# Kernel tuning notes

Hardware: AMD Instinct MI355X
Metric: run time of the kernel (lower is better)

## Reference

```python
import jax, jax.numpy as jnp
import numpy as np

BN_EPS = 1e-5

def conv1x1(x, w, b):
    # x: [N,C,T,V], w: [O,C], b: [O]
    return jnp.einsum('nctv,oc->notv', x, w) + b[None, :, None, None]

def conv9(x, w, b):
    # (9,1) temporal conv, padding (4,0). x: [N,C,T,V], w: [O,C,9], b: [O]
    out = jax.lax.conv_general_dilated(
        x, w[:, :, :, None], window_strides=(1, 1), padding=((4, 4), (0, 0)),
        dimension_numbers=('NCHW', 'OIHW', 'NCHW'))
    return out + b[None, :, None, None]

def attn_adj(f1, f2):
    # f1,f2: [N,inter,T,V] -> softmax over rows (axis -2) of [N,V,V]
    N, ic, T, V = f1.shape
    a1 = jnp.transpose(f1, (0, 3, 1, 2)).reshape(N, V, ic * T)  # permute(0,3,1,2).view
    a2 = f2.reshape(N, ic * T, V)
    scores = jnp.einsum('nvk,nkw->nvw', a1, a2) / (ic * T)
    return jax.nn.softmax(scores, axis=-2)


def setup_inputs() -> dict:
    key = jax.random.key(0)
    ks = jax.random.split(key, 16)
    N, C, T, V, S, IC = 16, 256, 64, 25, 3, 64
    s = lambda k, shape, sc=0.05: jax.random.normal(k, shape, dtype=jnp.float32) * sc
    return {
        'x': jax.random.normal(ks[0], (N, C, T, V), dtype=jnp.float32),
        'A': jax.random.uniform(ks[1], (S, V, V), dtype=jnp.float32),
        'PA': s(ks[2], (S, V, V), 1e-3),
        'wa': s(ks[3], (S, IC, C)), 'ba': jnp.zeros((S, IC), jnp.float32),
        'wb': s(ks[4], (S, IC, C)), 'bb': jnp.zeros((S, IC), jnp.float32),
        'wT1': s(ks[5], (S, IC, C, 9)), 'bT1': jnp.zeros((S, IC), jnp.float32),
        'wT2': s(ks[6], (S, IC, C, 9)), 'bT2': jnp.zeros((S, IC), jnp.float32),
        'wST11': s(ks[7], (S, IC, C, 9)), 'bST11': jnp.zeros((S, IC), jnp.float32),
        'wST12': s(ks[8], (S, IC, C, 9)), 'bST12': jnp.zeros((S, IC), jnp.float32),
        'wd': s(ks[9], (S, C, C)), 'bd': jnp.zeros((S, C), jnp.float32),
        'gamma': jnp.ones((C,), jnp.float32), 'beta': jnp.zeros((C,), jnp.float32),
        'bn_mean': jnp.zeros((C,), jnp.float32), 'bn_var': jnp.ones((C,), jnp.float32),
    }


def reference(x, A, PA, wa, ba, wb, bb, wT1, bT1, wT2, bT2,
              wST11, bST11, wST12, bST12, wd, bd, gamma, beta, bn_mean, bn_var):
    N, C, T, V = x.shape
    I = jnp.eye(V, dtype=x.dtype)
    # Chebyshev-like static graph transforms (computed once in __init__ in torch)
    A_ch4s = jax.nn.softmax((8 * A**4 - 4 * A**2 - 4 * A + I) / V, axis=-2)
    A_ch3 = 4 * A**2 - A - 2 * I
    A_all = A_ch3 + A_ch4s + PA  # [3,V,V]

    xf = x.reshape(N, C * T, V)
    y = 0.0
    for i in range(3):
        A1 = attn_adj(conv1x1(x, wa[i], ba[i]), conv1x1(x, wb[i], bb[i]))
        AT = attn_adj(conv9(x, wT1[i], bT1[i]), conv9(x, wT2[i], bT2[i]))
        # ModuleList append quirk: even i -> 1x1 conv (center tap), odd i -> (9,1) conv
        if i % 2 == 0:
            s1 = conv1x1(x, wST11[i, :, :, 4], bST11[i])
            s2 = conv1x1(x, wST12[i, :, :, 4], bST12[i])
        else:
            s1 = conv9(x, wST11[i], bST11[i])
            s2 = conv9(x, wST12[i], bST12[i])
        AST = attn_adj(s1, s2)
        Ai = A_all[i] + A1 + AT + AST  # [N,V,V]
        z = jnp.einsum('nkv,nvw->nkw', xf, Ai).reshape(N, C, T, V)
        y = y + conv1x1(z, wd[i], bd[i])

    yb = (y - bn_mean[None, :, None, None]) * (gamma[None, :, None, None]
         / jnp.sqrt(bn_var[None, :, None, None] + BN_EPS)) + beta[None, :, None, None]
    return jax.nn.relu(yb + x)  # down is identity (in_channels == out_channels)
```

## Files before the change

kernel.cpp:

```cpp
#include <hip/hip_runtime.h>
#include <hip/hip_bf16.h>

#define NN 16
#define CC 256
#define TT 64
#define VV 25
#define ICC 64
#define TV 1600
#define CTV 409600
#define NICTV 1638400

typedef __bf16 v8bf __attribute__((ext_vector_type(8)));
typedef __bf16 v4bf __attribute__((ext_vector_type(4)));
typedef float f32x16 __attribute__((ext_vector_type(16)));

struct ConvPairs {
  const __bf16* wA[5];
  const __bf16* wB[5];
  const float*  bA[5];
  const float*  bB[5];
};

__device__ __forceinline__ void gl_lds16(const __bf16* g, __bf16* l){
  __builtin_amdgcn_global_load_lds(
      (const __attribute__((address_space(1))) unsigned int*)g,
      (__attribute__((address_space(3))) unsigned int*)l, 16, 0, 0);
}

__global__ __launch_bounds__(256) void prep_k(
    const float* __restrict__ x, __bf16* __restrict__ xt,
    const float* __restrict__ wT1, const float* __restrict__ wT2,
    const float* __restrict__ wST11, const float* __restrict__ wST12,
    __bf16* __restrict__ wT1p, __bf16* __restrict__ wT2p,
    __bf16* __restrict__ wS1p, __bf16* __restrict__ wS2p,
    const float* __restrict__ wa, const float* __restrict__ wb,
    __bf16* __restrict__ wabp, __bf16* __restrict__ wScp,
    const float* __restrict__ wd, __bf16* __restrict__ wdb,
    const float* __restrict__ A, const float* __restrict__ PA,
    float* __restrict__ Aall, __bf16* __restrict__ zp){
  __shared__ __align__(16) float smf[64*65];
  __bf16* smb = (__bf16*)smf;
  int b = blockIdx.x;
  int tid = threadIdx.x;
  if (b < 64){
    int t = b >> 3, ch64 = (b >> 1) & 3, o2 = b & 1;
    const float* src; __bf16* dst;
    if (t < 3)      { src = wT1  + (size_t)t*147456;     dst = wT1p + (size_t)t*147456; }
    else if (t < 6) { src = wT2  + (size_t)(t-3)*147456; dst = wT2p + (size_t)(t-3)*147456; }
    else if (t == 6){ src = wST11 + 147456;              dst = wS1p; }
    else            { src = wST12 + 147456;              dst = wS2p; }
    const float* in = src + (size_t)(o2*32)*2304 + ch64*576;
    for (int i = tid; i < 32*576; i += 256){
      int row = i / 576, cc = i % 576;
      smb[i] = (__bf16)in[(size_t)row*2304 + cc];
    }
    __syncthreads();
    for (int i = tid; i < 18432; i += 256){
      int e = i & 7, l = (i >> 3) & 63, ks = (i >> 9) & 1;
      int r10 = i >> 10;
      int tap = r10 % 9, chh = r10 / 9;
      int ol = l & 31, hh = l >> 5;
      int cl = ks*16 + hh*8 + e;
      int c64 = chh*32 + cl;
      int ch8 = ch64*2 + chh;
      dst[(size_t)((((ch8*9 + tap)*2 + ks)*2 + o2)*512) + l*8 + e]
          = smb[ol*576 + c64*9 + tap];
    }
  } else if (b < 74){
    int u = b - 64;
    for (int it = 0; it < 8; ++it){
      int i = tid + it*256;
      int e = i & 7, l = (i >> 3) & 63, o2 = (i >> 9) & 1;
      int ks = (i >> 10) & 1, ch = i >> 11;
      int ol = l & 31, hh = l >> 5;
      int o = o2*32 + ol;
      int c = ch*32 + ks*16 + hh*8 + e;
      __bf16 v;
      if (u < 6){
        const float* w = (u < 3) ? (wa + (size_t)u*16384) : (wb + (size_t)(u-3)*16384);
        v = (__bf16)w[(size_t)o*256 + c];
      } else {
        int i9 = ((u == 6) || (u == 8)) ? 0 : 2;
        const float* w = ((u < 8) ? wST11 : wST12) + (size_t)i9*147456;
        v = (__bf16)w[((size_t)o*256 + c)*9 + 4];
      }
      __bf16* dst = (u < 6) ? (wabp + (size_t)u*16384) : (wScp + (size_t)(u-6)*16384);
      dst[i] = v;
    }
  } else if (b < 842){
    int i = (b-74)*256 + tid;
    if (i < 196608) wdb[i] = (__bf16)wd[i];
  } else if (b == 842){
    int t = tid;
    if (t < 75){
      int s = t / 25, w = t % 25;
      float a[25], m[25];
      float mx = -3.4e38f;
      for (int v = 0; v < 25; ++v){
        float av = A[(s*25 + v)*25 + w];
        a[v] = av;
        float d = (v == w) ? 1.f : 0.f;
        float mm = (8.f*av*av*av*av - 4.f*av*av - 4.f*av + d) * 0.04f;
        m[v] = mm;
        mx = fmaxf(mx, mm);
      }
      float sum = 0.f;
      for (int v = 0; v < 25; ++v){ float e = __expf(m[v]-mx); m[v] = e; sum += e; }
      float inv = 1.f/sum;
      for (int v = 0; v < 25; ++v){
        float av = a[v];
        float d = (v == w) ? 1.f : 0.f;
        Aall[(s*25+v)*25 + w] = m[v]*inv + 4.f*av*av - av - 2.f*d + PA[(s*25+v)*25+w];
      }
    } else if (t >= 128){
      zp[t-128] = (__bf16)0.f;
    }
  } else {
    int idx = b - 843;
    int p0 = (idx % 25)*64, c0 = ((idx/25) & 3)*64, n = idx/100;
    for (int i = tid; i < 4096; i += 256){
      int cc = i >> 6, pp = i & 63;
      smf[cc*65+pp] = x[(size_t)n*CTV + (size_t)(c0+cc)*TV + p0 + pp];
    }
    __syncthreads();
    for (int i = tid; i < 4096; i += 256){
      int pp = i >> 6, cc = i & 63;
      xt[((size_t)n*TV + p0+pp)*256 + c0+cc] = (__bf16)smf[cc*65+pp];
    }
  }
}

template<int NTAPS>
__global__ __launch_bounds__(512, 2) void conv13_k(const __bf16* __restrict__ xt,
    ConvPairs cp, const __bf16* __restrict__ zp, __bf16* __restrict__ fbuf){
  extern __shared__ __bf16 sm[];
  constexpr int HALO  = (NTAPS==9) ? 100 : 0;
  constexpr int NROWS = 512 + 2*HALO;
  constexpr int SLOTS = NROWS*4;
  constexpr int KSTG  = (SLOTS + 511)/512;
  constexpr int NSTEP = NTAPS*2;
  constexpr int AD    = (NSTEP >= 4) ? 4 : 2;
  int p0 = blockIdx.x*512;
  int n  = blockIdx.y;
  int pr = blockIdx.z;
  int tid = threadIdx.x;
  int lane = tid & 63;
  int wave = tid >> 6;
  int which = wave >> 2, wq = wave & 3;
  int h = lane >> 5, l31 = lane & 31;
  const __bf16* wp = (which ? cp.wB[pr] : cp.wA[pr]) + lane*8;
  const __bf16* xtn = xt + (size_t)n*CTV;
  __bf16* buf0 = sm;
  __bf16* buf1 = sm + NROWS*32;

  f32x16 acc[2][4];
  #pragma unroll
  for (int a=0;a<2;++a)
    #pragma unroll
    for (int b=0;b<4;++b)
      #pragma unroll
      for (int r=0;r<16;++r) acc[a][b][r] = 0.f;

  int rowbase = wq*128 + l31;

  auto stage = [&](__bf16* bn, int ch){
    #pragma unroll
    for (int k=0; k<KSTG; ++k){
      int slot = k*512 + tid;
      if ((SLOTS & 511) && slot >= SLOTS) continue;
      const __bf16* src;
      if (NTAPS == 1){
        int l31s = slot & 31, f = slot >> 5;
        int h_ = f & 1, ks_ = (f >> 1) & 1, pblk = f >> 2;
        int pg = p0 + pblk*32 + l31s;
        src = (pg < 1600) ? (xtn + (size_t)pg*256 + ch*32 + ks_*16 + h_*8)
                          : zp;
      } else {
        int row = slot >> 2, g2 = slot & 3;
        int g = (g2 - (row>>1)) & 3;
        int pg = p0 - HALO + row;
        src = ((unsigned)pg < 1600u) ? (xtn + (size_t)pg*256 + ch*32 + g*8)
                                     : zp;
      }
      gl_lds16(src, bn + (size_t)slot*8);
    }
  };
  auto ldA = [&](int ch, int s, v8bf* aa){
    int tap = s >> 1, ks = s & 1;
    size_t o = (size_t)(((ch*NTAPS + tap)*2 + ks)*2)*512;
    aa[0] = *(const v8bf*)(wp + o);
    aa[1] = *(const v8bf*)(wp + o + 512);
  };
  auto ldB = [&](const __bf16* bc, int s, v8bf* bb){
    int tap = s >> 1, ks = s & 1;
    #pragma unroll
    for (int pq=0; pq<4; ++pq){
      if (NTAPS == 1){
        int frag = ((wq*4 + pq)*2 + ks)*2 + h;
        bb[pq] = *(const v8bf*)(bc + frag*256 + l31*8);
      } else {
        int row = tap*25 + rowbase + pq*32;
        int gs = ((ks*2 + h) + (row>>1)) & 3;
        bb[pq] = *(const v8bf*)(bc + row*32 + gs*8);
      }
    }
  };

  v8bf ar[AD][2];
  #pragma unroll
  for (int i=0; i<AD; ++i) ldA(0, i, ar[i]);
  stage(buf0, 0);
  __syncthreads();

  for (int ch=0; ch<8; ++ch){
    const __bf16* bc = (ch & 1) ? buf1 : buf0;
    __bf16*       bn = (ch & 1) ? buf0 : buf1;
    if (ch < 7) stage(bn, ch+1);
    v8bf bR[2][4];
    ldB(bc, 0, bR[0]);
    ldB(bc, 1, bR[1]);
    #pragma unroll
    for (int s=0; s<NSTEP; ++s){
      int cb = s & 1;
      int ca = s & (AD-1);
      v8bf A0 = ar[ca][0], A1 = ar[ca][1];
      v8bf B0 = bR[cb][0], B1 = bR[cb][1], B2 = bR[cb][2], B3 = bR[cb][3];
      if (s+2 < NSTEP) ldB(bc, s+2, bR[cb]);
      if (s+AD < NSTEP)      ldA(ch, s+AD, ar[ca]);
      else if (ch < 7)       ldA(ch+1, s+AD-NSTEP, ar[ca]);
      __builtin_amdgcn_s_setprio(1);
      acc[0][0] = __builtin_amdgcn_mfma_f32_32x32x16_bf16(A0, B0, acc[0][0], 0,0,0);
      acc[1][0] = __builtin_amdgcn_mfma_f32_32x32x16_bf16(A1, B0, acc[1][0], 0,0,0);
      acc[0][1] = __builtin_amdgcn_mfma_f32_32x32x16_bf16(A0, B1, acc[0][1], 0,0,0);
      acc[1][1] = __builtin_amdgcn_mfma_f32_32x32x16_bf16(A1, B1, acc[1][1], 0,0,0);
      acc[0][2] = __builtin_amdgcn_mfma_f32_32x32x16_bf16(A0, B2, acc[0][2], 0,0,0);
      acc[1][2] = __builtin_amdgcn_mfma_f32_32x32x16_bf16(A1, B2, acc[1][2], 0,0,0);
      acc[0][3] = __builtin_amdgcn_mfma_f32_32x32x16_bf16(A0, B3, acc[0][3], 0,0,0);
      acc[1][3] = __builtin_amdgcn_mfma_f32_32x32x16_bf16(A1, B3, acc[1][3], 0,0,0);
      __builtin_amdgcn_s_setprio(0);
    }
    __syncthreads();
  }

  const float* bias = which ? cp.bB[pr] : cp.bA[pr];
  __bf16* outb = fbuf + (size_t)(pr*2 + which)*NICTV + (size_t)n*TV*64;
  #pragma unroll
  for (int pq=0; pq<4; ++pq){
    int p = p0 + wq*128 + pq*32 + l31;
    if (p >= 1600) continue;
    __bf16* orow = outb + (size_t)p*64;
    #pragma unroll
    for (int of=0; of<2; ++of){
      #pragma unroll
      for (int g=0; g<4; ++g){
        int og = of*32 + 8*g + 4*h;
        v4bf pk;
        #pragma unroll
        for (int j=0;j<4;++j) pk[j] = (__bf16)(acc[of][pq][4*g+j] + bias[og+j]);
        *(v4bf*)(orow + og) = pk;
      }
    }
  }
}

__global__ __launch_bounds__(256, 2) void ugemm6_k(const __bf16* __restrict__ xt,
    const __bf16* __restrict__ wdb, __bf16* __restrict__ ubuf){
  __shared__ __bf16 sm[64*256];
  int p0 = blockIdx.x*64;
  int n  = blockIdx.y;
  int tid = threadIdx.x;
  int lane = tid & 63;
  int os = tid >> 6;
  int h = lane >> 5, l31 = lane & 31;
  const __bf16* xtn = xt + (size_t)n*CTV;

  for (int s2 = tid; s2 < 64*32; s2 += 256){
    int row = s2 >> 5, g = s2 & 31;
    uint4 val = *(const uint4*)(xtn + (size_t)(p0+row)*256 + g*8);
    int gs = (g + row) & 31;
    *(uint4*)(sm + row*256 + gs*8) = val;
  }
  __syncthreads();

  auto ldB = [&](int ks, v8bf* bb){
    #pragma unroll
    for (int pq=0; pq<2; ++pq){
      int row = pq*32 + l31;
      int gs = ((ks*2 + h) + row) & 31;
      bb[pq] = *(const v8bf*)(sm + row*256 + gs*8);
    }
  };

  for (int br=0; br<3; ++br){
    const __bf16* wl = wdb + ((size_t)br*256 + os*64 + l31)*256 + h*8;
    auto ldA = [&](int ks, v8bf& A0, v8bf& A1){
      A0 = *(const v8bf*)(wl + ks*16);
      A1 = *(const v8bf*)(wl + (size_t)32*256 + ks*16);
    };
    f32x16 acc[2][2];
    #pragma unroll
    for (int a=0;a<2;++a)
      #pragma unroll
      for (int b=0;b<2;++b)
        #pragma unroll
        for (int r=0;r<16;++r) acc[a][b][r] = 0.f;

    v8bf a0[4], a1[4];
    ldA(0, a0[0], a1[0]);
    ldA(1, a0[1], a1[1]);
    ldA(2, a0[2], a1[2]);
    ldA(3, a0[3], a1[3]);
    v8bf bR[2][2];
    ldB(0, bR[0]);
    ldB(1, bR[1]);
    #pragma unroll
    for (int ks=0; ks<16; ++ks){
      int c2 = ks & 1, cur = ks & 3;
      v8bf B0 = bR[c2][0], B1 = bR[c2][1];
      v8bf A0 = a0[cur], A1 = a1[cur];
      if (ks+2 < 16) ldB(ks+2, bR[c2]);
      if (ks+4 < 16) ldA(ks+4, a0[cur], a1[cur]);
      acc[0][0] = __builtin_amdgcn_mfma_f32_32x32x16_bf16(A0, B0, acc[0][0], 0,0,0);
      acc[1][0] = __builtin_amdgcn_mfma_f32_32x32x16_bf16(A1, B0, acc[1][0], 0,0,0);
      acc[0][1] = __builtin_amdgcn_mfma_f32_32x32x16_bf16(A0, B1, acc[0][1], 0,0,0);
      acc[1][1] = __builtin_amdgcn_mfma_f32_32x32x16_bf16(A1, B1, acc[1][1], 0,0,0);
    }

    #pragma unroll
    for (int pq=0; pq<2; ++pq){
      int p = p0 + pq*32 + l31;
      __bf16* out = ubuf + ((size_t)(br*NN + n)*TV + p)*256;
      #pragma unroll
      for (int oq=0; oq<2; ++oq){
        #pragma unroll
        for (int g=0; g<4; ++g){
          int og = os*64 + oq*32 + 8*g + 4*h;
          v4bf pk;
          #pragma unroll
          for (int j=0;j<4;++j) pk[j] = (__bf16)acc[oq][pq][4*g+j];
          *(v4bf*)(out + og) = pk;
        }
      }
    }
  }
}

__global__ __launch_bounds__(256) void scores_m_k(const __bf16* __restrict__ fbuf,
                                                  float* __restrict__ part, int pairbase){
  int n = blockIdx.y, pr = blockIdx.z;
  int tid = threadIdx.x;
  int lane = tid & 63;
  int wave = tid >> 6;
  int chunk = blockIdx.x*4 + wave;
  int h = lane >> 5, l31 = lane & 31;
  const __bf16* f1 = fbuf + (size_t)(pr*2)*NICTV   + (size_t)n*TV*64;
  const __bf16* f2 = fbuf + (size_t)(pr*2+1)*NICTV + (size_t)n*TV*64;
  int t0 = chunk*4;

  f32x16 acc;
  #pragma unroll
  for (int r=0;r<16;++r) acc[r] = 0.f;

  auto off = [&](int s)->size_t{
    int t = t0 + (s>>2), og = s&3;
    return ((size_t)(t*25 + l31))*64 + og*16 + h*8;
  };
  v8bf A[4], B[4];
  #pragma unroll
  for (int i=0; i<4; ++i){
    size_t o = off(i);
    A[i] = *(const v8bf*)(f1+o); B[i] = *(const v8bf*)(f2+o);
  }
  #pragma unroll
  for (int s=0; s<16; ++s){
    int cur = s & 3;
    v8bf Ac = A[cur], Bc = B[cur];
    if (s+4 < 16){
      size_t o2 = off(s+4);
      A[cur] = *(const v8bf*)(f1+o2);
      B[cur] = *(const v8bf*)(f2+o2);
    }
    acc = __builtin_amdgcn_mfma_f32_32x32x16_bf16(Ac, Bc, acc, 0,0,0);
  }

  size_t tile = (((size_t)(pairbase+pr)*NN + n)*16 + chunk);
  float* pt = part + tile*1024;
  #pragma unroll
  for (int r=0; r<16; ++r){
    int row = (r&3) + 8*(r>>2) + 4*h;
    pt[row*32 + l31] = acc[r];
  }
}

__global__ __launch_bounds__(64) void reduce_all_k(const float* __restrict__ part,
    const float* __restrict__ Aall, float* __restrict__ Ai3){
  const int pairbr[9] = {0,1,2,0,2, 0,1,2,1};
  int n = blockIdx.x, w = blockIdx.y;
  int lane = threadIdx.x;
  float accbr[3] = {0.f, 0.f, 0.f};
  for (int pr=0; pr<9; ++pr){
    float s = 0.f;
    if (lane < 25){
      const float* pp = part + (((size_t)pr*NN + n)*16)*1024 + lane*32 + w;
      #pragma unroll
      for (int ch=0; ch<16; ++ch) s += pp[(size_t)ch*1024];
    }
    s *= (1.f/4096.f);
    float mval = (lane<25) ? s : -3.4e38f;
    #pragma unroll
    for (int d=32; d>0; d>>=1) mval = fmaxf(mval, __shfl_xor(mval, d));
    float e = (lane<25) ? __expf(s - mval) : 0.f;
    float sum = e;
    #pragma unroll
    for (int d=32; d>0; d>>=1) sum += __shfl_xor(sum, d);
    accbr[pairbr[pr]] += e / sum;
  }
  if (lane < 25){
    #pragma unroll
    for (int br=0; br<3; ++br)
      Ai3[((size_t)br*NN + n)*625 + lane*25 + w] =
        Aall[br*625 + lane*25 + w] + accbr[br];
  }
}

__global__ __launch_bounds__(256) void yep_k(const float* __restrict__ x,
    const float* __restrict__ Ai3, const __bf16* __restrict__ ubuf,
    const float* __restrict__ bd, const float* __restrict__ gamma,
    const float* __restrict__ beta, const float* __restrict__ bnm,
    const float* __restrict__ bnv, float* __restrict__ out){
  __shared__ float ais[3][25*28];
  int t = blockIdx.x, n = blockIdx.y, o = threadIdx.x;
  for (int l=o; l<2100; l+=256){
    int br = l/700, r = l%700;
    int v = r/28, w = r%28;
    ais[br][v*28+w] = (w<25) ? Ai3[((size_t)br*NN + n)*625 + v*25 + w] : 0.f;
  }
  __syncthreads();
  float y[28];
  #pragma unroll
  for (int w=0;w<28;++w) y[w]=0.f;
  for (int br=0; br<3; ++br){
    const __bf16* up = ubuf + ((size_t)(br*NN + n)*TV + t*25)*256 + o;
    float uv[25];
    #pragma unroll
    for (int v=0;v<25;++v) uv[v] = (float)up[(size_t)v*256];
    const float* ab = ais[br];
    for (int v=0; v<25; ++v){
      float u = uv[v];
      #pragma unroll
      for (int j=0; j<7; ++j){
        float4 a4 = *(const float4*)(ab + v*28 + 4*j);
        y[4*j+0] = fmaf(u, a4.x, y[4*j+0]);
        y[4*j+1] = fmaf(u, a4.y, y[4*j+1]);
        y[4*j+2] = fmaf(u, a4.z, y[4*j+2]);
        y[4*j+3] = fmaf(u, a4.w, y[4*j+3]);
      }
    }
  }
  float bsum = bd[o] + bd[256+o] + bd[512+o];
  float sc = gamma[o] * rsqrtf(bnv[o] + 1e-5f);
  float m  = bnm[o], be = beta[o];
  const float* xr = x + (size_t)n*CTV + (size_t)o*TV + t*25;
  float* orow = out + (size_t)n*CTV + (size_t)o*TV + t*25;
  #pragma unroll
  for (int w=0; w<25; ++w)
    orow[w] = fmaxf((y[w] + bsum - m)*sc + be + xr[w], 0.f);
}

extern "C" void kernel_launch(void* const* d_in, const int* in_sizes, int n_in,
                              void* d_out, int out_size, void* d_ws, size_t ws_size,
                              hipStream_t stream) {
  const float* x     = (const float*)d_in[0];
  const float* A     = (const float*)d_in[1];
  const float* PA    = (const float*)d_in[2];
  const float* wa    = (const float*)d_in[3];
  const float* ba    = (const float*)d_in[4];
  const float* wb    = (const float*)d_in[5];
  const float* bb    = (const float*)d_in[6];
  const float* wT1   = (const float*)d_in[7];
  const float* bT1   = (const float*)d_in[8];
  const float* wT2   = (const float*)d_in[9];
  const float* bT2   = (const float*)d_in[10];
  const float* wST11 = (const float*)d_in[11];
  const float* bST11 = (const float*)d_in[12];
  const float* wST12 = (const float*)d_in[13];
  const float* bST12 = (const float*)d_in[14];
  const float* wd    = (const float*)d_in[15];
  const float* bd    = (const float*)d_in[16];
  const float* gamma = (const float*)d_in[17];
  const float* beta  = (const float*)d_in[18];
  const float* bnm   = (const float*)d_in[19];
  const float* bnv   = (const float*)d_in[20];

  char* W = (char*)d_ws;
  float*  Aall = (float*)W;  W += 8192;
  __bf16* zp   = (__bf16*)W; W += 256;
  float*  Ai3  = (float*)W;  W += 122880;
  __bf16* wabp = (__bf16*)W; W += 196608;
  __bf16* wScp = (__bf16*)W; W += 131072;
  __bf16* wT1p = (__bf16*)W; W += 884736;
  __bf16* wT2p = (__bf16*)W; W += 884736;
  __bf16* wS1p = (__bf16*)W; W += 294912;
  __bf16* wS2p = (__bf16*)W; W += 294912;
  __bf16* wdb  = (__bf16*)W; W += 393216;
  __bf16* xt   = (__bf16*)W; W += 13107200;
  char* R = W;               W += 39321600;
  float*  part = (float*)W;  W += 9437184;
  __bf16* fbuf = (__bf16*)R;
  __bf16* ubuf = (__bf16*)R;

  prep_k<<<2443, 256, 0, stream>>>(x, xt, wT1, wT2, wST11, wST12,
                                   wT1p, wT2p, wS1p, wS2p,
                                   wa, wb, wabp, wScp, wd, wdb, A, PA, Aall, zp);

  {
    ConvPairs cp;
    for (int i=0;i<3;++i){
      cp.wA[i] = wabp + (size_t)i*16384;      cp.wB[i] = wabp + (size_t)(3+i)*16384;
      cp.bA[i] = ba + i*64;                   cp.bB[i] = bb + i*64;
    }
    int evens[2] = {0, 2};
    for (int j=0;j<2;++j){
      int i = evens[j];
      cp.wA[3+j] = wScp + (size_t)j*16384;    cp.wB[3+j] = wScp + (size_t)(2+j)*16384;
      cp.bA[3+j] = bST11 + i*64;              cp.bB[3+j] = bST12 + i*64;
    }
    conv13_k<1><<<dim3(4,16,5), 512, 2*512*32*2, stream>>>(xt, cp, zp, fbuf);
    scores_m_k<<<dim3(4,16,5), 256, 0, stream>>>(fbuf, part, 0);
  }

  {
    ConvPairs cp;
    for (int i=0;i<3;++i){
      cp.wA[i] = wT1p + (size_t)i*147456;  cp.wB[i] = wT2p + (size_t)i*147456;
      cp.bA[i] = bT1 + i*64;               cp.bB[i] = bT2 + i*64;
    }
    cp.wA[3] = wS1p;  cp.wB[3] = wS2p;
    cp.bA[3] = bST11 + 64;  cp.bB[3] = bST12 + 64;
    cp.wA[4] = cp.wA[3]; cp.wB[4] = cp.wB[3]; cp.bA[4] = cp.bA[3]; cp.bB[4] = cp.bB[3];
    conv13_k<9><<<dim3(4,16,4), 512, 2*712*32*2, stream>>>(xt, cp, zp, fbuf);
    scores_m_k<<<dim3(4,16,4), 256, 0, stream>>>(fbuf, part, 5);
  }

  ugemm6_k<<<dim3(25,16), 256, 0, stream>>>(xt, wdb, ubuf);
  reduce_all_k<<<dim3(16,25), 64, 0, stream>>>(part, Aall, Ai3);
  yep_k<<<dim3(64,16), 256, 0, stream>>>(x, Ai3, ubuf, bd, gamma, beta, bnm, bnv,
                                         (float*)d_out);
}
```

Baseline: 358.3 us.

## Restructure conv MFMA loop into phased load/compute with interleaved chunk staging

Replaces the per-step rolling register prefetch of A/B fragments with a phased schedule. Each phase loads a batch of A and B fragments, issues one chunk of the next channel's global-to-LDS staging, and then runs a block of MFMAs between raw s_barriers. The intent is to spread the async LDS staging across phases and give the MFMA stream fewer interleaved memory waits. The cost is more barriers per channel and more live registers per phase (SPP=3 for the 9-tap kernel), which may lower occupancy or expose load latency.

```diff
diff --git a/kernel.cpp b/kernel.cpp
--- a/kernel.cpp
+++ b/kernel.cpp
@@ -131,15 +131,16 @@
 }
 
 template<int NTAPS>
-__global__ __launch_bounds__(512, 2) void conv13_k(const __bf16* __restrict__ xt,
+__global__ __launch_bounds__(512, 2) void conv18_k(const __bf16* __restrict__ xt,
     ConvPairs cp, const __bf16* __restrict__ zp, __bf16* __restrict__ fbuf){
   extern __shared__ __bf16 sm[];
   constexpr int HALO  = (NTAPS==9) ? 100 : 0;
   constexpr int NROWS = 512 + 2*HALO;
   constexpr int SLOTS = NROWS*4;
-  constexpr int KSTG  = (SLOTS + 511)/512;
+  constexpr int CHUNKS= (SLOTS + 511)/512;
   constexpr int NSTEP = NTAPS*2;
-  constexpr int AD    = (NSTEP >= 4) ? 4 : 2;
+  constexpr int PH    = (NTAPS==9) ? 6 : 1;
+  constexpr int SPP   = NSTEP/PH;
   int p0 = blockIdx.x*512;
   int n  = blockIdx.y;
   int pr = blockIdx.z;
@@ -163,11 +164,9 @@
 
   int rowbase = wq*128 + l31;
 
-  auto stage = [&](__bf16* bn, int ch){
-    #pragma unroll
-    for (int k=0; k<KSTG; ++k){
-      int slot = k*512 + tid;
-      if ((SLOTS & 511) && slot >= SLOTS) continue;
+  auto stageChunk = [&](__bf16* bn, int ch, int k){
+    int slot = k*512 + tid;
+    if (slot < SLOTS){
       const __bf16* src;
       if (NTAPS == 1){
         int l31s = slot & 31, f = slot >> 5;
@@ -206,40 +205,46 @@
     }
   };
 
-  v8bf ar[AD][2];
-  #pragma unroll
-  for (int i=0; i<AD; ++i) ldA(0, i, ar[i]);
-  stage(buf0, 0);
-  __syncthreads();
+  #pragma unroll
+  for (int k=0; k<CHUNKS; ++k) stageChunk(buf0, 0, k);
+  asm volatile("s_waitcnt vmcnt(0)" ::: "memory");
+  __builtin_amdgcn_s_barrier();
 
   for (int ch=0; ch<8; ++ch){
     const __bf16* bc = (ch & 1) ? buf1 : buf0;
     __bf16*       bn = (ch & 1) ? buf0 : buf1;
-    if (ch < 7) stage(bn, ch+1);
-    v8bf bR[2][4];
-    ldB(bc, 0, bR[0]);
-    ldB(bc, 1, bR[1]);
-    #pragma unroll
-    for (int s=0; s<NSTEP; ++s){
-      int cb = s & 1;
-      int ca = s & (AD-1);
-      v8bf A0 = ar[ca][0], A1 = ar[ca][1];
-      v8bf B0 = bR[cb][0], B1 = bR[cb][1], B2 = bR[cb][2], B3 = bR[cb][3];
-      if (s+2 < NSTEP) ldB(bc, s+2, bR[cb]);
-      if (s+AD < NSTEP)      ldA(ch, s+AD, ar[ca]);
-      else if (ch < 7)       ldA(ch+1, s+AD-NSTEP, ar[ca]);
+    #pragma unroll
+    for (int ph=0; ph<PH; ++ph){
+      v8bf ar[SPP][2], br[SPP][4];
+      #pragma unroll
+      for (int s3=0; s3<SPP; ++s3) ldA(ch, ph*SPP + s3, ar[s3]);
+      #pragma unroll
+      for (int s3=0; s3<SPP; ++s3) ldB(bc, ph*SPP + s3, br[s3]);
+      if (ch < 7){
+        if (NTAPS == 9) stageChunk(bn, ch+1, ph);
+        else {
+          #pragma unroll
+          for (int k=0; k<CHUNKS; ++k) stageChunk(bn, ch+1, k);
+        }
+      }
+      __builtin_amdgcn_s_barrier();
+      __builtin_amdgcn_sched_barrier(0);
       __builtin_amdgcn_s_setprio(1);
-      acc[0][0] = __builtin_amdgcn_mfma_f32_32x32x16_bf16(A0, B0, acc[0][0], 0,0,0);
-      acc[1][0] = __builtin_amdgcn_mfma_f32_32x32x16_bf16(A1, B0, acc[1][0], 0,0,0);
-      acc[0][1] = __builtin_amdgcn_mfma_f32_32x32x16_bf16(A0, B1, acc[0][1], 0,0,0);
-      acc[1][1] = __builtin_amdgcn_mfma_f32_32x32x16_bf16(A1, B1, acc[1][1], 0,0,0);
-      acc[0][2] = __builtin_amdgcn_mfma_f32_32x32x16_bf16(A0, B2, acc[0][2], 0,0,0);
-      acc[1][2] = __builtin_amdgcn_mfma_f32_32x32x16_bf16(A1, B2, acc[1][2], 0,0,0);
-      acc[0][3] = __builtin_amdgcn_mfma_f32_32x32x16_bf16(A0, B3, acc[0][3], 0,0,0);
-      acc[1][3] = __builtin_amdgcn_mfma_f32_32x32x16_bf16(A1, B3, acc[1][3], 0,0,0);
+      #pragma unroll
+      for (int s3=0; s3<SPP; ++s3){
+        v8bf A0 = ar[s3][0], A1 = ar[s3][1];
+        #pragma unroll
+        for (int pq=0; pq<4; ++pq){
+          acc[0][pq] = __builtin_amdgcn_mfma_f32_32x32x16_bf16(A0, br[s3][pq], acc[0][pq], 0,0,0);
+          acc[1][pq] = __builtin_amdgcn_mfma_f32_32x32x16_bf16(A1, br[s3][pq], acc[1][pq], 0,0,0);
+        }
+      }
       __builtin_amdgcn_s_setprio(0);
-    }
-    __syncthreads();
+      if (ph == PH-1){
+        asm volatile("s_waitcnt vmcnt(0)" ::: "memory");
+      }
+      __builtin_amdgcn_s_barrier();
+    }
   }
 
   const float* bias = which ? cp.bB[pr] : cp.bA[pr];
@@ -525,7 +530,7 @@
       cp.wA[3+j] = wScp + (size_t)j*16384;    cp.wB[3+j] = wScp + (size_t)(2+j)*16384;
       cp.bA[3+j] = bST11 + i*64;              cp.bB[3+j] = bST12 + i*64;
     }
-    conv13_k<1><<<dim3(4,16,5), 512, 2*512*32*2, stream>>>(xt, cp, zp, fbuf);
+    conv18_k<1><<<dim3(4,16,5), 512, 2*512*32*2, stream>>>(xt, cp, zp, fbuf);
     scores_m_k<<<dim3(4,16,5), 256, 0, stream>>>(fbuf, part, 0);
   }
 
@@ -538,7 +543,7 @@
     cp.wA[3] = wS1p;  cp.wB[3] = wS2p;
     cp.bA[3] = bST11 + 64;  cp.bB[3] = bST12 + 64;
     cp.wA[4] = cp.wA[3]; cp.wB[4] = cp.wB[3]; cp.bA[4] = cp.bA[3]; cp.bB[4] = cp.bB[3];
-    conv13_k<9><<<dim3(4,16,4), 512, 2*712*32*2, stream>>>(xt, cp, zp, fbuf);
+    conv18_k<9><<<dim3(4,16,4), 512, 2*712*32*2, stream>>>(xt, cp, zp, fbuf);
     scores_m_k<<<dim3(4,16,4), 256, 0, stream>>>(fbuf, part, 5);
   }
 
```

Measured after the change: 363.1 us. No clear change (+1.3%).
